# Kernel tuning notes

Measured on AMD Instinct MI355X. Metric: run time of the kernel, lower is better.

## Reference

```python
import jax, jax.numpy as jnp
import numpy as np

B, N, M, D = 64, 197, 65, 768


def setup_inputs() -> dict:
    key = jax.random.key(0)
    k1, k2, k3 = jax.random.split(key, 3)
    image = jax.random.normal(k1, (B, N, D), dtype=jnp.float32)
    text = jax.random.normal(k2, (B, M, D), dtype=jnp.float32)
    pm = jax.random.randint(k3, (B, M), 0, 2).astype(jnp.int32)
    pm = pm.at[:, :2].set(0)  # CLS + first real token always valid
    logit_scale = jnp.ones((), dtype=jnp.float32)
    return {"image": image, "text": text, "padding_masks": pm, "logit_scale": logit_scale}


def _ce_with_diag_labels(logits):
    # F.cross_entropy(logits, arange(B)): mean of -log_softmax diag
    return -jnp.mean(jnp.diagonal(jax.nn.log_softmax(logits, axis=-1)))


def reference(image, text, padding_masks, logit_scale):
    # include_cls_token=False: original computes full [B,B,N,M] then slices
    # [:, :, 1:, 1:]; we compute the sliced tokens directly (same math).
    img = image[:, 1:, :]                   # [B, N-1, D]
    txt = text[:, 1:, :]                    # [B, M-1, D]
    pm = padding_masks[:, 1:].astype(bool)  # [B, M-1] True = padded

    # sim[i,j,n,m] = logit_scale * <img_i,n , txt_j,m>
    sim = logit_scale * jnp.einsum('ind,jmd->ijnm', img, txt)  # [B,B,N-1,M-1]

    # Original masks with NaN along mask of batch-row i (broadcast over j,n).
    # logits_per_image: nan_to_num(-inf) -> max over m -> mean over n
    sim_img = jnp.where(pm[:, None, None, :], -jnp.inf, sim)
    logits_per_image = jnp.mean(jnp.max(sim_img, axis=3), axis=2)  # [B,B]

    # logits_per_text: max over n (NaN cols stay NaN) -> nanmean over m.
    # Equivalent masked mean over valid m (mask constant along n).
    max_n = jnp.max(sim, axis=2)                         # [B,B,M-1]
    valid = ~pm                                          # [B,M-1]
    cnt = jnp.sum(valid, axis=1).astype(sim.dtype)       # [B]
    logits_per_text = jnp.sum(
        jnp.where(valid[:, None, :], max_n, 0.0), axis=2
    ) / cnt[:, None]                                     # [B,B]

    loss = 0.5 * (_ce_with_diag_labels(logits_per_image)
                  + _ce_with_diag_labels(logits_per_text))
    targets = jnp.arange(logits_per_image.shape[0], dtype=jnp.int32)
    return loss, logits_per_image, logits_per_text, targets
```

## Files before the change

### kernel.cpp

```cpp
#include <hip/hip_runtime.h>

typedef _Float16 half8 __attribute__((ext_vector_type(8)));
typedef float floatx4 __attribute__((ext_vector_type(4)));
typedef float float4v __attribute__((ext_vector_type(4)));

#define DIM   768
#define NROW  196
#define AUNITS (64 * 13 * 24 * 64)
#define TUNITS (64 * 4 * 24 * 64)
#define A_HALFS ((size_t)AUNITS * 8)
#define BJ_HALFS (24 * 4 * 64 * 8)
#define CHUNK_H 8192

__device__ __forceinline__ void gl_lds16(const _Float16* g, _Float16* l) {
  __builtin_amdgcn_global_load_lds(
      (const __attribute__((address_space(1))) unsigned int*)g,
      (__attribute__((address_space(3))) unsigned int*)l, 16, 0, 0);
}

__global__ __launch_bounds__(256) void repack(const float* __restrict__ img,
                                              const float* __restrict__ txt,
                                              _Float16* __restrict__ Apk,
                                              _Float16* __restrict__ Bpk) {
  int gid = blockIdx.x * 256 + threadIdx.x;
  const float* src;
  _Float16* dst;
  if (gid < AUNITS) {
    int l = gid & 63, g = gid >> 6;
    int s = g % 24; g /= 24;
    int tau = g % 13; int i = g / 13;
    int n = tau * 16 + (l & 15); if (n > 195) n = 195;
    src = img + (size_t)i * 197 * 768 + (size_t)(n + 1) * 768 + s * 32 + (l >> 4) * 8;
    dst = Apk + (size_t)gid * 8;
  } else {
    int u = gid - AUNITS;
    int l = u & 63, g = u >> 6;
    int ct = g & 3; g >>= 2;
    int s = g % 24; int j = g / 24;
    int m = ct * 16 + (l & 15);
    src = txt + (size_t)j * 65 * 768 + (size_t)(m + 1) * 768 + s * 32 + (l >> 4) * 8;
    dst = Bpk + (size_t)u * 8;
  }
  float4v v0 = *(const float4v*)src;
  float4v v1 = *(const float4v*)(src + 4);
  half8 h;
  h[0] = (_Float16)v0[0]; h[1] = (_Float16)v0[1]; h[2] = (_Float16)v0[2]; h[3] = (_Float16)v0[3];
  h[4] = (_Float16)v1[0]; h[5] = (_Float16)v1[1]; h[6] = (_Float16)v1[2]; h[7] = (_Float16)v1[3];
  *(half8*)dst = h;
}

__global__ __launch_bounds__(256, 3) void sim_kernel(const _Float16* __restrict__ Apk,
                                                     const _Float16* __restrict__ Bpk,
                                                     const int* __restrict__ pm,
                                                     const float* __restrict__ ls,
                                                     float* __restrict__ lpi,
                                                     float* __restrict__ lpt) {
  __shared__ _Float16 Bsh[2 * CHUNK_H];

  const int j = blockIdx.x, i = blockIdx.y;
  const int tid = threadIdx.x;
  const int wave = tid >> 6, lane = tid & 63;
  const int r16 = lane & 15;
  const int lane8 = lane * 8;

  const _Float16* Ai = Apk + (size_t)i * 13 * 24 * 512;
  const _Float16* pA[4];
  pA[0] = Ai + (size_t)(wave)     * 24 * 512 + lane8;
  pA[1] = Ai + (size_t)(wave + 4) * 24 * 512 + lane8;
  pA[2] = Ai + (size_t)(wave + 8) * 24 * 512 + lane8;
  pA[3] = Ai + (size_t)12         * 24 * 512 + lane8;
  const _Float16* Bg = Bpk + (size_t)j * BJ_HALFS;

#pragma unroll
  for (int r = 0; r < 4; ++r) {
    int u = wave * 4 + r;
    gl_lds16(Bg + u * 512 + lane8, Bsh + u * 512);
  }

  half8 af[2][4];
#pragma unroll
  for (int d = 0; d < 2; ++d)
#pragma unroll
    for (int t = 0; t < 4; ++t)
      af[d][t] = *(const half8*)(pA[t] + d * 512);

  floatx4 acc[3][4];
  floatx4 acc12 = (floatx4){0.f, 0.f, 0.f, 0.f};
#pragma unroll
  for (int t = 0; t < 3; ++t)
#pragma unroll
    for (int cc = 0; cc < 4; ++cc)
      acc[t][cc] = (floatx4){0.f, 0.f, 0.f, 0.f};

#pragma unroll
  for (int c = 0; c < 6; ++c) {
    __syncthreads();
#pragma unroll
    for (int sc = 0; sc < 4; ++sc) {
      const int s = c * 4 + sc;
      if (sc == 2 && c < 5) {
#pragma unroll
        for (int r = 0; r < 4; ++r) {
          int u = wave * 4 + r;
          gl_lds16(Bg + (c + 1) * CHUNK_H + u * 512 + lane8,
                   Bsh + ((c + 1) & 1) * CHUNK_H + u * 512);
        }
      }
      half8 bfr[4];
#pragma unroll
      for (int cc = 0; cc < 4; ++cc) {
        int ct = (wave + cc) & 3;
        bfr[cc] = *(const half8*)(Bsh + (c & 1) * CHUNK_H + (sc * 4 + ct) * 512 + lane8);
      }
      half8 a0 = af[s & 1][0], a1 = af[s & 1][1], a2 = af[s & 1][2], a3 = af[s & 1][3];
      if (s < 22) {
#pragma unroll
        for (int t = 0; t < 4; ++t) af[s & 1][t] = *(const half8*)(pA[t] + (s + 2) * 512);
      }
#pragma unroll
      for (int cc = 0; cc < 4; ++cc) {
        acc[0][cc] = __builtin_amdgcn_mfma_f32_16x16x32_f16(a0, bfr[cc], acc[0][cc], 0, 0, 0);
        acc[1][cc] = __builtin_amdgcn_mfma_f32_16x16x32_f16(a1, bfr[cc], acc[1][cc], 0, 0, 0);
        acc[2][cc] = __builtin_amdgcn_mfma_f32_16x16x32_f16(a2, bfr[cc], acc[2][cc], 0, 0, 0);
      }
      acc12 = __builtin_amdgcn_mfma_f32_16x16x32_f16(a3, bfr[0], acc12, 0, 0, 0);
    }
  }

  const float sgl = ls[0];
  bool msk[4];
  int colc[4];
#pragma unroll
  for (int cc = 0; cc < 4; ++cc) {
    colc[cc] = ((wave + cc) & 3) * 16 + r16;
    msk[cc] = pm[i * 65 + 1 + colc[cc]] != 0;
  }

  float rowsum = 0.f;
#pragma unroll
  for (int t = 0; t < 3; ++t) {
#pragma unroll
    for (int r = 0; r < 4; ++r) {
      float rm = -__builtin_inff();
#pragma unroll
      for (int cc = 0; cc < 4; ++cc) {
        float v = acc[t][cc][r] * sgl;
        rm = fmaxf(rm, msk[cc] ? -__builtin_inff() : v);
      }
#pragma unroll
      for (int off = 1; off < 16; off <<= 1)
        rm = fmaxf(rm, __shfl_xor(rm, off, 64));
      rowsum += rm;
    }
  }
#pragma unroll
  for (int off = 1; off < 64; off <<= 1) rowsum += __shfl_xor(rowsum, off, 64);

  float cmv[4];
#pragma unroll
  for (int cc = 0; cc < 4; ++cc) {
    float cm = -__builtin_inff();
#pragma unroll
    for (int t = 0; t < 3; ++t)
#pragma unroll
      for (int r = 0; r < 4; ++r)
        cm = fmaxf(cm, acc[t][cc][r] * sgl);
    cm = fmaxf(cm, __shfl_xor(cm, 16, 64));
    cm = fmaxf(cm, __shfl_xor(cm, 32, 64));
    cmv[cc] = cm;
  }

  __syncthreads();
  float* colmaxLDS = (float*)Bsh;
  float* t12buf    = (float*)Bsh + 256;
  float* wsumLDS   = (float*)Bsh + 512;

  if (lane == 0) wsumLDS[wave] = rowsum;
  if (lane < 16) {
#pragma unroll
    for (int cc = 0; cc < 4; ++cc) colmaxLDS[wave * 64 + colc[cc]] = cmv[cc];
#pragma unroll
    for (int r = 0; r < 4; ++r) t12buf[r * 64 + wave * 16 + r16] = acc12[r] * sgl;
  }
  __syncthreads();

  if (tid < 64) {
    int col = tid;
    bool valid = pm[i * 65 + 1 + col] == 0;
    float t0 = t12buf[col], t1 = t12buf[64 + col], t2 = t12buf[128 + col], t3 = t12buf[192 + col];
    float v = fmaxf(fmaxf(colmaxLDS[col], colmaxLDS[64 + col]),
                    fmaxf(colmaxLDS[128 + col], colmaxLDS[192 + col]));
    v = fmaxf(v, fmaxf(fmaxf(t0, t1), fmaxf(t2, t3)));
    float contrib = valid ? v : 0.f;
    float cntv = valid ? 1.f : 0.f;
    float rs0 = valid ? t0 : -__builtin_inff();
    float rs1 = valid ? t1 : -__builtin_inff();
    float rs2 = valid ? t2 : -__builtin_inff();
    float rs3 = valid ? t3 : -__builtin_inff();
#pragma unroll
    for (int off = 1; off < 64; off <<= 1) {
      contrib += __shfl_xor(contrib, off, 64);
      cntv += __shfl_xor(cntv, off, 64);
      rs0 = fmaxf(rs0, __shfl_xor(rs0, off, 64));
      rs1 = fmaxf(rs1, __shfl_xor(rs1, off, 64));
      rs2 = fmaxf(rs2, __shfl_xor(rs2, off, 64));
      rs3 = fmaxf(rs3, __shfl_xor(rs3, off, 64));
    }
    if (tid == 0) {
      lpt[i * 64 + j] = contrib / cntv;
      float wtot = wsumLDS[0] + wsumLDS[1] + wsumLDS[2] + wsumLDS[3];
      lpi[i * 64 + j] = (wtot * 0.0625f + rs0 + rs1 + rs2 + rs3) / 196.f;
    }
  }
}

__global__ __launch_bounds__(64) void ce_kernel(float* __restrict__ out) {
  const int t = threadIdx.x;
  const float* lpi = out + 1;
  const float* lpt = out + 1 + 4096;

  float mx = -__builtin_inff();
  for (int jj = 0; jj < 64; ++jj) mx = fmaxf(mx, lpi[t * 64 + jj]);
  float se = 0.f;
  for (int jj = 0; jj < 64; ++jj) se += __expf(lpi[t * 64 + jj] - mx);
  float ci = (mx + __logf(se)) - lpi[t * 64 + t];

  float mx2 = -__builtin_inff();
  for (int jj = 0; jj < 64; ++jj) mx2 = fmaxf(mx2, lpt[t * 64 + jj]);
  float se2 = 0.f;
  for (int jj = 0; jj < 64; ++jj) se2 += __expf(lpt[t * 64 + jj] - mx2);
  float ct_ = (mx2 + __logf(se2)) - lpt[t * 64 + t];

  float v = ci + ct_;
#pragma unroll
  for (int off = 1; off < 64; off <<= 1) v += __shfl_xor(v, off, 64);
  if (t == 0) out[0] = 0.5f * v / 64.f;
  out[1 + 8192 + t] = (float)t;
}

extern "C" void kernel_launch(void* const* d_in, const int* in_sizes, int n_in,
                              void* d_out, int out_size, void* d_ws, size_t ws_size,
                              hipStream_t stream) {
  const float* image = (const float*)d_in[0];
  const float* text  = (const float*)d_in[1];
  const int*   pm    = (const int*)d_in[2];
  const float* ls    = (const float*)d_in[3];
  float* out = (float*)d_out;

  _Float16* Apk = (_Float16*)d_ws;
  _Float16* Bpk = Apk + A_HALFS;

  repack<<<(AUNITS + TUNITS) / 256, 256, 0, stream>>>(image, text, Apk, Bpk);

  dim3 grid(64, 64);
  sim_kernel<<<grid, 256, 0, stream>>>(Apk, Bpk, pm, ls, out + 1, out + 1 + 4096);
  ce_kernel<<<1, 64, 0, stream>>>(out);
}
```

Baseline: 203.8 us.

## Compute two text batches per block to reuse image fragments

Each block now handles two j (text) batches instead of one, halving the grid and loading each image A-fragment once for twice the MFMA work. The LDS buffer doubles to hold two B tiles per chunk, and the B prefetch moves to the start of each chunk. Accumulators double, so the occupancy hint drops from 3 to 2 blocks per CU. This trades occupancy and register pressure for less global A traffic.

```diff
diff --git a/kernel.cpp b/kernel.cpp
--- a/kernel.cpp
+++ b/kernel.cpp
@@ -10,7 +10,6 @@
 #define TUNITS (64 * 4 * 24 * 64)
 #define A_HALFS ((size_t)AUNITS * 8)
 #define BJ_HALFS (24 * 4 * 64 * 8)
-#define CHUNK_H 8192
 
 __device__ __forceinline__ void gl_lds16(const _Float16* g, _Float16* l) {
   __builtin_amdgcn_global_load_lds(
@@ -49,15 +48,15 @@
   *(half8*)dst = h;
 }
 
-__global__ __launch_bounds__(256, 3) void sim_kernel(const _Float16* __restrict__ Apk,
+__global__ __launch_bounds__(256, 2) void sim_kernel(const _Float16* __restrict__ Apk,
                                                      const _Float16* __restrict__ Bpk,
                                                      const int* __restrict__ pm,
                                                      const float* __restrict__ ls,
                                                      float* __restrict__ lpi,
                                                      float* __restrict__ lpt) {
-  __shared__ _Float16 Bsh[2 * CHUNK_H];
-
-  const int j = blockIdx.x, i = blockIdx.y;
+  __shared__ _Float16 Bsh[32768];
+
+  const int jb = blockIdx.x, i = blockIdx.y;
   const int tid = threadIdx.x;
   const int wave = tid >> 6, lane = tid & 63;
   const int r16 = lane & 15;
@@ -69,12 +68,14 @@
   pA[1] = Ai + (size_t)(wave + 4) * 24 * 512 + lane8;
   pA[2] = Ai + (size_t)(wave + 8) * 24 * 512 + lane8;
   pA[3] = Ai + (size_t)12         * 24 * 512 + lane8;
-  const _Float16* Bg = Bpk + (size_t)j * BJ_HALFS;
-
-#pragma unroll
-  for (int r = 0; r < 4; ++r) {
-    int u = wave * 4 + r;
-    gl_lds16(Bg + u * 512 + lane8, Bsh + u * 512);
+  const _Float16* Bg = Bpk + (size_t)(2 * jb) * BJ_HALFS;
+
+#pragma unroll
+  for (int r8 = 0; r8 < 8; ++r8) {
+    int u = wave * 8 + r8;
+    int jj = u >> 4, rr = u & 15;
+    gl_lds16(Bg + (size_t)jj * BJ_HALFS + rr * 512 + lane8,
+             Bsh + jj * 8192 + rr * 512);
   }
 
   half8 af[2][4];
@@ -84,33 +85,40 @@
     for (int t = 0; t < 4; ++t)
       af[d][t] = *(const half8*)(pA[t] + d * 512);
 
-  floatx4 acc[3][4];
-  floatx4 acc12 = (floatx4){0.f, 0.f, 0.f, 0.f};
-#pragma unroll
-  for (int t = 0; t < 3; ++t)
-#pragma unroll
-    for (int cc = 0; cc < 4; ++cc)
-      acc[t][cc] = (floatx4){0.f, 0.f, 0.f, 0.f};
+  floatx4 acc[2][3][4];
+  floatx4 acc12[2];
+  acc12[0] = (floatx4){0.f, 0.f, 0.f, 0.f};
+  acc12[1] = (floatx4){0.f, 0.f, 0.f, 0.f};
+#pragma unroll
+  for (int jj = 0; jj < 2; ++jj)
+#pragma unroll
+    for (int t = 0; t < 3; ++t)
+#pragma unroll
+      for (int cc = 0; cc < 4; ++cc)
+        acc[jj][t][cc] = (floatx4){0.f, 0.f, 0.f, 0.f};
 
 #pragma unroll
   for (int c = 0; c < 6; ++c) {
     __syncthreads();
+    if (c < 5) {
+#pragma unroll
+      for (int r8 = 0; r8 < 8; ++r8) {
+        int u = wave * 8 + r8;
+        int jj = u >> 4, rr = u & 15;
+        gl_lds16(Bg + (size_t)jj * BJ_HALFS + (c + 1) * 8192 + rr * 512 + lane8,
+                 Bsh + ((c + 1) & 1) * 16384 + jj * 8192 + rr * 512);
+      }
+    }
 #pragma unroll
     for (int sc = 0; sc < 4; ++sc) {
       const int s = c * 4 + sc;
-      if (sc == 2 && c < 5) {
-#pragma unroll
-        for (int r = 0; r < 4; ++r) {
-          int u = wave * 4 + r;
-          gl_lds16(Bg + (c + 1) * CHUNK_H + u * 512 + lane8,
-                   Bsh + ((c + 1) & 1) * CHUNK_H + u * 512);
-        }
-      }
-      half8 bfr[4];
+      const int base = (c & 1) * 16384 + sc * 2048 + lane8;
+      half8 b0[4], b1[4];
 #pragma unroll
       for (int cc = 0; cc < 4; ++cc) {
         int ct = (wave + cc) & 3;
-        bfr[cc] = *(const half8*)(Bsh + (c & 1) * CHUNK_H + (sc * 4 + ct) * 512 + lane8);
+        b0[cc] = *(const half8*)(Bsh + base + ct * 512);
+        b1[cc] = *(const half8*)(Bsh + base + 8192 + ct * 512);
       }
       half8 a0 = af[s & 1][0], a1 = af[s & 1][1], a2 = af[s & 1][2], a3 = af[s & 1][3];
       if (s < 22) {
@@ -119,11 +127,15 @@
       }
 #pragma unroll
       for (int cc = 0; cc < 4; ++cc) {
-        acc[0][cc] = __builtin_amdgcn_mfma_f32_16x16x32_f16(a0, bfr[cc], acc[0][cc], 0, 0, 0);
-        acc[1][cc] = __builtin_amdgcn_mfma_f32_16x16x32_f16(a1, bfr[cc], acc[1][cc], 0, 0, 0);
-        acc[2][cc] = __builtin_amdgcn_mfma_f32_16x16x32_f16(a2, bfr[cc], acc[2][cc], 0, 0, 0);
-      }
-      acc12 = __builtin_amdgcn_mfma_f32_16x16x32_f16(a3, bfr[0], acc12, 0, 0, 0);
+        acc[0][0][cc] = __builtin_amdgcn_mfma_f32_16x16x32_f16(a0, b0[cc], acc[0][0][cc], 0, 0, 0);
+        acc[0][1][cc] = __builtin_amdgcn_mfma_f32_16x16x32_f16(a1, b0[cc], acc[0][1][cc], 0, 0, 0);
+        acc[0][2][cc] = __builtin_amdgcn_mfma_f32_16x16x32_f16(a2, b0[cc], acc[0][2][cc], 0, 0, 0);
+        acc[1][0][cc] = __builtin_amdgcn_mfma_f32_16x16x32_f16(a0, b1[cc], acc[1][0][cc], 0, 0, 0);
+        acc[1][1][cc] = __builtin_amdgcn_mfma_f32_16x16x32_f16(a1, b1[cc], acc[1][1][cc], 0, 0, 0);
+        acc[1][2][cc] = __builtin_amdgcn_mfma_f32_16x16x32_f16(a2, b1[cc], acc[1][2][cc], 0, 0, 0);
+      }
+      acc12[0] = __builtin_amdgcn_mfma_f32_16x16x32_f16(a3, b0[0], acc12[0], 0, 0, 0);
+      acc12[1] = __builtin_amdgcn_mfma_f32_16x16x32_f16(a3, b1[0], acc12[1], 0, 0, 0);
     }
   }
 
@@ -136,60 +148,68 @@
     msk[cc] = pm[i * 65 + 1 + colc[cc]] != 0;
   }
 
-  float rowsum = 0.f;
-#pragma unroll
-  for (int t = 0; t < 3; ++t) {
-#pragma unroll
-    for (int r = 0; r < 4; ++r) {
-      float rm = -__builtin_inff();
-#pragma unroll
-      for (int cc = 0; cc < 4; ++cc) {
-        float v = acc[t][cc][r] * sgl;
-        rm = fmaxf(rm, msk[cc] ? -__builtin_inff() : v);
-      }
-#pragma unroll
-      for (int off = 1; off < 16; off <<= 1)
-        rm = fmaxf(rm, __shfl_xor(rm, off, 64));
-      rowsum += rm;
-    }
-  }
-#pragma unroll
-  for (int off = 1; off < 64; off <<= 1) rowsum += __shfl_xor(rowsum, off, 64);
-
-  float cmv[4];
-#pragma unroll
-  for (int cc = 0; cc < 4; ++cc) {
-    float cm = -__builtin_inff();
-#pragma unroll
-    for (int t = 0; t < 3; ++t)
-#pragma unroll
-      for (int r = 0; r < 4; ++r)
-        cm = fmaxf(cm, acc[t][cc][r] * sgl);
-    cm = fmaxf(cm, __shfl_xor(cm, 16, 64));
-    cm = fmaxf(cm, __shfl_xor(cm, 32, 64));
-    cmv[cc] = cm;
+  float rowsum[2] = {0.f, 0.f};
+  float cmv[2][4];
+#pragma unroll
+  for (int jj = 0; jj < 2; ++jj) {
+#pragma unroll
+    for (int t = 0; t < 3; ++t) {
+#pragma unroll
+      for (int r = 0; r < 4; ++r) {
+        float rm = -__builtin_inff();
+#pragma unroll
+        for (int cc = 0; cc < 4; ++cc) {
+          float v = acc[jj][t][cc][r] * sgl;
+          rm = fmaxf(rm, msk[cc] ? -__builtin_inff() : v);
+        }
+#pragma unroll
+        for (int off = 1; off < 16; off <<= 1)
+          rm = fmaxf(rm, __shfl_xor(rm, off, 64));
+        rowsum[jj] += rm;
+      }
+    }
+#pragma unroll
+    for (int off = 1; off < 64; off <<= 1) rowsum[jj] += __shfl_xor(rowsum[jj], off, 64);
+
+#pragma unroll
+    for (int cc = 0; cc < 4; ++cc) {
+      float cm = -__builtin_inff();
+#pragma unroll
+      for (int t = 0; t < 3; ++t)
+#pragma unroll
+        for (int r = 0; r < 4; ++r)
+          cm = fmaxf(cm, acc[jj][t][cc][r] * sgl);
+      cm = fmaxf(cm, __shfl_xor(cm, 16, 64));
+      cm = fmaxf(cm, __shfl_xor(cm, 32, 64));
+      cmv[jj][cc] = cm;
+    }
   }
 
   __syncthreads();
-  float* colmaxLDS = (float*)Bsh;
-  float* t12buf    = (float*)Bsh + 256;
-  float* wsumLDS   = (float*)Bsh + 512;
-
-  if (lane == 0) wsumLDS[wave] = rowsum;
+  float* colmaxS = (float*)Bsh;
+  float* t12S    = (float*)Bsh + 512;
+  float* wsumS   = (float*)Bsh + 1024;
+
+  if (lane == 0) { wsumS[wave] = rowsum[0]; wsumS[4 + wave] = rowsum[1]; }
   if (lane < 16) {
 #pragma unroll
-    for (int cc = 0; cc < 4; ++cc) colmaxLDS[wave * 64 + colc[cc]] = cmv[cc];
-#pragma unroll
-    for (int r = 0; r < 4; ++r) t12buf[r * 64 + wave * 16 + r16] = acc12[r] * sgl;
+    for (int jj = 0; jj < 2; ++jj) {
+#pragma unroll
+      for (int cc = 0; cc < 4; ++cc) colmaxS[jj * 256 + wave * 64 + colc[cc]] = cmv[jj][cc];
+#pragma unroll
+      for (int r = 0; r < 4; ++r) t12S[jj * 256 + r * 64 + wave * 16 + r16] = acc12[jj][r] * sgl;
+    }
   }
   __syncthreads();
 
-  if (tid < 64) {
-    int col = tid;
+  if (tid < 128) {
+    const int jj = wave;
+    const int col = lane;
     bool valid = pm[i * 65 + 1 + col] == 0;
-    float t0 = t12buf[col], t1 = t12buf[64 + col], t2 = t12buf[128 + col], t3 = t12buf[192 + col];
-    float v = fmaxf(fmaxf(colmaxLDS[col], colmaxLDS[64 + col]),
-                    fmaxf(colmaxLDS[128 + col], colmaxLDS[192 + col]));
+    const float* cm = colmaxS + jj * 256;
+    const float* t12 = t12S + jj * 256;
+    float t0 = t12[col], t1 = t12[64 + col], t2 = t12[128 + col], t3 = t12[192 + col];
+    float v = fmaxf(fmaxf(cm[col], cm[64 + col]), fmaxf(cm[128 + col], cm[192 + col]));
     v = fmaxf(v, fmaxf(fmaxf(t0, t1), fmaxf(t2, t3)));
     float contrib = valid ? v : 0.f;
     float cntv = valid ? 1.f : 0.f;
@@ -206,10 +226,11 @@
       rs2 = fmaxf(rs2, __shfl_xor(rs2, off, 64));
       rs3 = fmaxf(rs3, __shfl_xor(rs3, off, 64));
     }
-    if (tid == 0) {
-      lpt[i * 64 + j] = contrib / cntv;
-      float wtot = wsumLDS[0] + wsumLDS[1] + wsumLDS[2] + wsumLDS[3];
-      lpi[i * 64 + j] = (wtot * 0.0625f + rs0 + rs1 + rs2 + rs3) / 196.f;
+    if (lane == 0) {
+      int jout = 2 * jb + jj;
+      lpt[i * 64 + jout] = contrib / cntv;
+      float wtot = wsumS[jj * 4 + 0] + wsumS[jj * 4 + 1] + wsumS[jj * 4 + 2] + wsumS[jj * 4 + 3];
+      lpi[i * 64 + jout] = (wtot * 0.0625f + rs0 + rs1 + rs2 + rs3) / 196.f;
     }
   }
 }
@@ -252,7 +273,7 @@
 
   repack<<<(AUNITS + TUNITS) / 256, 256, 0, stream>>>(image, text, Apk, Bpk);
 
-  dim3 grid(64, 64);
+  dim3 grid(32, 64);
   sim_kernel<<<grid, 256, 0, stream>>>(Apk, Bpk, pm, ls, out + 1, out + 1 + 4096);
   ce_kernel<<<1, 64, 0, stream>>>(out);
 }
```

Result: faster. 188.2 us (-7.7%).
